# Optimization experiments

Measured on AMD Instinct MI355X. Metric: run time of the kernel, lower is better.

The kernel has to match this reference:

```python
import jax, jax.numpy as jnp
import numpy as np

BLOCK = 8  # block_size init kwarg


def _process_block(block):
    """Serial Floyd-Steinberg error diffusion within one (BLOCK, BLOCK) tile."""
    def row_step(next_row_err, row):
        row = row + next_row_err  # add errors diffused from the row above
        def px_step(err_right, px):
            old = px + err_right
            new = jnp.where(old > 127.0, 255.0, 0.0)
            e = old - new
            return e * (7.0 / 16.0), (new, e)
        _, (new_row, errs) = jax.lax.scan(px_step, jnp.zeros((), row.dtype), row)
        z = jnp.zeros((1,), errs.dtype)
        # error at x goes to next row at x-1 (3/16), x (5/16), x+1 (1/16)
        nxt = (5.0 / 16.0) * errs \
            + (3.0 / 16.0) * jnp.concatenate([errs[1:], z]) \
            + (1.0 / 16.0) * jnp.concatenate([z, errs[:-1]])
        return nxt, new_row
    _, out = jax.lax.scan(row_step, jnp.zeros((block.shape[1],), block.dtype), block)
    return out


def _halftone(gray):
    """gray: (N, H, W) float32 in [0,255], H and W multiples of BLOCK."""
    N, H, W = gray.shape
    hb, wb = H // BLOCK, W // BLOCK
    blocks = gray.reshape(N, hb, BLOCK, wb, BLOCK).transpose(0, 1, 3, 2, 4)
    blocks = blocks.reshape(N * hb * wb, BLOCK, BLOCK)
    out = jax.vmap(_process_block)(blocks)
    out = out.reshape(N, hb, wb, BLOCK, BLOCK).transpose(0, 1, 3, 2, 4)
    return out.reshape(N, H, W)


def setup_inputs() -> dict:
    key = jax.random.key(0)
    batch = jax.random.uniform(key, (8, 3, 1024, 1024), dtype=jnp.float32)
    return {"batch": batch}


def reference(batch):
    scaled = batch * 255.0  # (B, 3, H, W)
    # cv2.COLOR_BGR2GRAY coefficients on channels [0,1,2] = [B,G,R]
    gray = 0.114 * scaled[:, 0] + 0.587 * scaled[:, 1] + 0.299 * scaled[:, 2]  # (B,H,W)
    # original swapaxes(0,2) -> halftoning runs on a (W, H) layout
    ht = _halftone(gray.transpose(0, 2, 1)).transpose(0, 2, 1)  # (B,H,W), values 0/255
    out = jnp.broadcast_to(ht[:, None, :, :], scaled.shape)
    out = jnp.where(scaled == 0.0, 0.0, out)  # mask: zero input stays zero
    return out / 255.0
```

## Files before the change

kernel.cpp:

```cpp
#include <hip/hip_runtime.h>
#include <stdint.h>


#define IMG_H 1024
#define IMG_W 1024
#define NCH   3

typedef uint32_t u32x4 __attribute__((ext_vector_type(4)));

__device__ __forceinline__ float bload(u32x4 rsrc, uint32_t voff_bytes) {
    float r;
    asm volatile("buffer_load_dword %0, %1, %2, 0 offen"
                 : "=v"(r) : "v"(voff_bytes), "s"(rsrc));
    return r;
}

__global__ __launch_bounds__(256, 6)
void fs_halftone_kernel(const float* __restrict__ in, float* __restrict__ out,
                        int n_imgs) {
#pragma clang fp contract(off)
    const int tiles_w = IMG_W / 8;
    const int tiles_per_img = tiles_w * (IMG_H / 8);

    int gtid = blockIdx.x * blockDim.x + threadIdx.x;
    int tile = gtid >> 3;
    int col  = gtid & 7;
    int lane = threadIdx.x & 63;
    int b  = tile / tiles_per_img;
    if (b >= n_imgs) return;
    int t  = tile % tiles_per_img;
    int th = t / tiles_w;
    int tw = t % tiles_w;

    const size_t imgstride = (size_t)IMG_H * IMG_W;
    const size_t col_off   = (size_t)(th * 8) * IMG_W + (size_t)(tw * 8) + (size_t)col;
    float* obase = out + (size_t)b * NCH * imgstride + col_off;

    u32x4 rsrc;
    {
        uint64_t a = (uint64_t)(uintptr_t)in;
        rsrc.x = (uint32_t)a;
        rsrc.y = (uint32_t)(a >> 32);
        rsrc.z = 0xFFFFFFFFu;
        rsrc.w = 0x00020000u;
    }
    const uint32_t voff0 =
        (uint32_t)(((size_t)b * NCH * imgstride + col_off) * sizeof(float));

    float a0[8], a1[8], a2[8];
#pragma unroll
    for (int r = 0; r < 8; ++r)
        a0[r] = bload(rsrc, voff0 + (uint32_t)(0 * 4194304 + r * 4096));
#pragma unroll
    for (int r = 0; r < 8; ++r)
        a1[r] = bload(rsrc, voff0 + (uint32_t)(1 * 4194304 + r * 4096));
#pragma unroll
    for (int r = 0; r < 8; ++r)
        a2[r] = bload(rsrc, voff0 + (uint32_t)(2 * 4194304 + r * 4096));

    asm volatile("s_waitcnt vmcnt(0)" ::: "memory");
    __builtin_amdgcn_sched_barrier(0);

    float p[8];
    unsigned int zm0 = 0u, zm1 = 0u, zm2 = 0u;
#pragma unroll
    for (int r = 0; r < 8; ++r) {
        float s0 = a0[r] * 255.0f;
        float s1 = a1[r] * 255.0f;
        float s2 = a2[r] * 255.0f;
        if (s0 == 0.0f) zm0 |= 1u << r;
        if (s1 == 0.0f) zm1 |= 1u << r;
        if (s2 == 0.0f) zm2 |= 1u << r;
        p[r] = ((0.114f * s0) + (0.587f * s1)) + (0.299f * s2);
    }

    float nrow[8];
#pragma unroll
    for (int j = 0; j < 8; ++j) nrow[j] = 0.0f;

    unsigned int ob = 0u;

#pragma unroll
    for (int i = 0; i < 8; ++i) {
        float cv[8];
#pragma unroll
        for (int j = 0; j < 8; ++j)
            cv[j] = __shfl(p[j], (lane & ~7) | i);

        float errs[8];
        float er = 0.0f;
        unsigned int onb = 0u;
#pragma unroll
        for (int j = 0; j < 8; ++j) {
            float px  = cv[j] + nrow[j];
            float old = px + er;
            bool  on  = old > 127.0f;
            float nw  = on ? 255.0f : 0.0f;
            float e   = old - nw;
            er = e * 0.4375f;
            errs[j] = e;
            if (on) onb |= 1u << j;
        }
        if (col == i) ob = onb;
#pragma unroll
        for (int j = 0; j < 8; ++j) {
            float en = (j < 7) ? errs[j + 1] : 0.0f;
            float ep = (j > 0) ? errs[j - 1] : 0.0f;
            nrow[j] = ((0.3125f * errs[j]) + (0.1875f * en)) + (0.0625f * ep);
        }
    }

#pragma unroll
    for (int ch = 0; ch < 3; ++ch) {
        unsigned int zm = (ch == 0) ? zm0 : ((ch == 1) ? zm1 : zm2);
#pragma unroll
        for (int r = 0; r < 8; ++r) {
            bool on = (ob >> r) & 1u;
            bool z  = (zm >> r) & 1u;
            obase[ch * imgstride + (size_t)r * IMG_W] = (on && !z) ? 1.0f : 0.0f;
        }
    }
}

extern "C" void kernel_launch(void* const* d_in, const int* in_sizes, int n_in,
                              void* d_out, int out_size, void* d_ws, size_t ws_size,
                              hipStream_t stream) {
    const float* in  = (const float*)d_in[0];
    float*       out = (float*)d_out;

    int n_imgs = in_sizes[0] / (NCH * IMG_H * IMG_W);
    int total_threads = 8 * n_imgs * (IMG_H / 8) * (IMG_W / 8);
    int block = 256;
    int grid = (total_threads + block - 1) / block;
    fs_halftone_kernel<<<grid, block, 0, stream>>>(in, out, n_imgs);
}
```

Measured before the change: 38.71 us.

## Process two tiles per thread to overlap second tile's loads with compute

Measured after the change: 38.24 us. About the same (-1.2%).

```diff
diff --git a/kernel.cpp b/kernel.cpp
--- a/kernel.cpp
+++ b/kernel.cpp
@@ -15,54 +15,12 @@
     return r;
 }
 
-__global__ __launch_bounds__(256, 6)
-void fs_halftone_kernel(const float* __restrict__ in, float* __restrict__ out,
-                        int n_imgs) {
+__device__ __forceinline__ void gray_col(const float (&a0)[8], const float (&a1)[8],
+                                         const float (&a2)[8], float (&p)[8],
+                                         unsigned int& zm0, unsigned int& zm1,
+                                         unsigned int& zm2) {
 #pragma clang fp contract(off)
-    const int tiles_w = IMG_W / 8;
-    const int tiles_per_img = tiles_w * (IMG_H / 8);
-
-    int gtid = blockIdx.x * blockDim.x + threadIdx.x;
-    int tile = gtid >> 3;
-    int col  = gtid & 7;
-    int lane = threadIdx.x & 63;
-    int b  = tile / tiles_per_img;
-    if (b >= n_imgs) return;
-    int t  = tile % tiles_per_img;
-    int th = t / tiles_w;
-    int tw = t % tiles_w;
-
-    const size_t imgstride = (size_t)IMG_H * IMG_W;
-    const size_t col_off   = (size_t)(th * 8) * IMG_W + (size_t)(tw * 8) + (size_t)col;
-    float* obase = out + (size_t)b * NCH * imgstride + col_off;
-
-    u32x4 rsrc;
-    {
-        uint64_t a = (uint64_t)(uintptr_t)in;
-        rsrc.x = (uint32_t)a;
-        rsrc.y = (uint32_t)(a >> 32);
-        rsrc.z = 0xFFFFFFFFu;
-        rsrc.w = 0x00020000u;
-    }
-    const uint32_t voff0 =
-        (uint32_t)(((size_t)b * NCH * imgstride + col_off) * sizeof(float));
-
-    float a0[8], a1[8], a2[8];
-#pragma unroll
-    for (int r = 0; r < 8; ++r)
-        a0[r] = bload(rsrc, voff0 + (uint32_t)(0 * 4194304 + r * 4096));
-#pragma unroll
-    for (int r = 0; r < 8; ++r)
-        a1[r] = bload(rsrc, voff0 + (uint32_t)(1 * 4194304 + r * 4096));
-#pragma unroll
-    for (int r = 0; r < 8; ++r)
-        a2[r] = bload(rsrc, voff0 + (uint32_t)(2 * 4194304 + r * 4096));
-
-    asm volatile("s_waitcnt vmcnt(0)" ::: "memory");
-    __builtin_amdgcn_sched_barrier(0);
-
-    float p[8];
-    unsigned int zm0 = 0u, zm1 = 0u, zm2 = 0u;
+    zm0 = zm1 = zm2 = 0u;
 #pragma unroll
     for (int r = 0; r < 8; ++r) {
         float s0 = a0[r] * 255.0f;
@@ -73,20 +31,20 @@
         if (s2 == 0.0f) zm2 |= 1u << r;
         p[r] = ((0.114f * s0) + (0.587f * s1)) + (0.299f * s2);
     }
+}
 
+__device__ __forceinline__ unsigned int run_fs(const float (&p)[8], int lane, int col) {
+#pragma clang fp contract(off)
     float nrow[8];
 #pragma unroll
     for (int j = 0; j < 8; ++j) nrow[j] = 0.0f;
-
     unsigned int ob = 0u;
-
 #pragma unroll
     for (int i = 0; i < 8; ++i) {
         float cv[8];
 #pragma unroll
         for (int j = 0; j < 8; ++j)
             cv[j] = __shfl(p[j], (lane & ~7) | i);
-
         float errs[8];
         float er = 0.0f;
         unsigned int onb = 0u;
@@ -109,7 +67,13 @@
             nrow[j] = ((0.3125f * errs[j]) + (0.1875f * en)) + (0.0625f * ep);
         }
     }
+    return ob;
+}
 
+__device__ __forceinline__ void store_col(float* obase, unsigned int ob,
+                                          unsigned int zm0, unsigned int zm1,
+                                          unsigned int zm2) {
+    const size_t imgstride = (size_t)IMG_H * IMG_W;
 #pragma unroll
     for (int ch = 0; ch < 3; ++ch) {
         unsigned int zm = (ch == 0) ? zm0 : ((ch == 1) ? zm1 : zm2);
@@ -122,6 +86,79 @@
     }
 }
 
+__global__ __launch_bounds__(256, 5)
+void fs_halftone_kernel(const float* __restrict__ in, float* __restrict__ out,
+                        int n_imgs) {
+#pragma clang fp contract(off)
+    const int tiles_w = IMG_W / 8;
+    const int tiles_per_img = tiles_w * (IMG_H / 8);
+    const int total_tiles = n_imgs * tiles_per_img;
+    const int half = total_tiles >> 1;
+
+    int gtid = blockIdx.x * blockDim.x + threadIdx.x;
+    int pairid = gtid >> 3;
+    int col  = gtid & 7;
+    int lane = threadIdx.x & 63;
+    if (pairid >= half) return;
+
+    const size_t imgstride = (size_t)IMG_H * IMG_W;
+
+    auto tile_elem_off = [&](int T) -> size_t {
+        int b  = T / tiles_per_img;
+        int t  = T % tiles_per_img;
+        int th = t / tiles_w;
+        int tw = t % tiles_w;
+        return (size_t)b * NCH * imgstride + (size_t)(th * 8) * IMG_W
+             + (size_t)(tw * 8) + (size_t)col;
+    };
+    const size_t offA = tile_elem_off(pairid);
+    const size_t offB = tile_elem_off(pairid + half);
+
+    u32x4 rsrc;
+    {
+        uint64_t a = (uint64_t)(uintptr_t)in;
+        rsrc.x = (uint32_t)a;
+        rsrc.y = (uint32_t)(a >> 32);
+        rsrc.z = 0xFFFFFFFFu;
+        rsrc.w = 0x00020000u;
+    }
+    const uint32_t vA = (uint32_t)(offA * sizeof(float));
+    const uint32_t vB = (uint32_t)(offB * sizeof(float));
+
+    float a0[8], a1[8], a2[8], b0[8], b1[8], b2[8];
+#pragma unroll
+    for (int r = 0; r < 8; ++r) a0[r] = bload(rsrc, vA + (uint32_t)(0 * 4194304 + r * 4096));
+#pragma unroll
+    for (int r = 0; r < 8; ++r) a1[r] = bload(rsrc, vA + (uint32_t)(1 * 4194304 + r * 4096));
+#pragma unroll
+    for (int r = 0; r < 8; ++r) a2[r] = bload(rsrc, vA + (uint32_t)(2 * 4194304 + r * 4096));
+#pragma unroll
+    for (int r = 0; r < 8; ++r) b0[r] = bload(rsrc, vB + (uint32_t)(0 * 4194304 + r * 4096));
+#pragma unroll
+    for (int r = 0; r < 8; ++r) b1[r] = bload(rsrc, vB + (uint32_t)(1 * 4194304 + r * 4096));
+#pragma unroll
+    for (int r = 0; r < 8; ++r) b2[r] = bload(rsrc, vB + (uint32_t)(2 * 4194304 + r * 4096));
+
+    asm volatile("s_waitcnt vmcnt(24)" ::: "memory");
+    __builtin_amdgcn_sched_barrier(0);
+
+    float pA[8];
+    unsigned int zA0, zA1, zA2;
+    gray_col(a0, a1, a2, pA, zA0, zA1, zA2);
+    unsigned int obA = run_fs(pA, lane, col);
+
+    asm volatile("s_waitcnt vmcnt(0)" ::: "memory");
+    __builtin_amdgcn_sched_barrier(0);
+
+    store_col(out + offA, obA, zA0, zA1, zA2);
+
+    float pB[8];
+    unsigned int zB0, zB1, zB2;
+    gray_col(b0, b1, b2, pB, zB0, zB1, zB2);
+    unsigned int obB = run_fs(pB, lane, col);
+    store_col(out + offB, obB, zB0, zB1, zB2);
+}
+
 extern "C" void kernel_launch(void* const* d_in, const int* in_sizes, int n_in,
                               void* d_out, int out_size, void* d_ws, size_t ws_size,
                               hipStream_t stream) {
@@ -129,7 +166,9 @@
     float*       out = (float*)d_out;
 
     int n_imgs = in_sizes[0] / (NCH * IMG_H * IMG_W);
-    int total_threads = 8 * n_imgs * (IMG_H / 8) * (IMG_W / 8);
+    int total_tiles = n_imgs * (IMG_H / 8) * (IMG_W / 8);
+    int half = total_tiles / 2;
+    int total_threads = 8 * half;
     int block = 256;
     int grid = (total_threads + block - 1) / block;
     fs_halftone_kernel<<<grid, block, 0, stream>>>(in, out, n_imgs);
```
